# Kernel tuning notes

Hardware: AMD Instinct MI355X
Metric: run time of the kernel (lower is better)

## Reference

```python
import jax, jax.numpy as jnp
import numpy as np

SIG = [1, 1, 1, 1, -1]  # Cl(4,1)
NVEC = 5
GA = 1 << NVEC  # 32


def _build_gp_table():
    # Cayley table for the geometric product on blades indexed by bitmask.
    G = np.zeros((GA, GA, GA), np.float32)
    for a in range(GA):
        for b in range(GA):
            s = 0
            t = a >> 1
            while t:
                s += bin(t & b).count('1')
                t >>= 1
            sign = -1.0 if (s & 1) else 1.0
            common = a & b
            for i in range(NVEC):
                if (common >> i) & 1:
                    sign *= SIG[i]
            G[a, b, a ^ b] = sign
    return G

GP_TABLE = jnp.asarray(_build_gp_table())


def geometric_product(x, y):
    return jnp.einsum('...i,...j,ijk->...k', x, y, GP_TABLE)


def manifold_norm(x):
    # normalize each multivector onto the unit sphere in R^32
    return x / (jnp.linalg.norm(x, axis=-1, keepdims=True) + 1e-6)


def versor_linear(x, W, b):
    # channel mixing shared across multivector components: x [..., in, ga]
    return jnp.einsum('...ig,oi->...og', x, W) + b


def layer_norm2d(x, w, b):
    # LayerNorm over last two dims [D, ga] jointly
    mu = jnp.mean(x, axis=(-2, -1), keepdims=True)
    var = jnp.var(x, axis=(-2, -1), keepdims=True)
    return (x - mu) / jnp.sqrt(var + 1e-5) * w + b


def attention(x, Wq, bq, Wk, bk, Wv, bv, Wo, bo, n_heads):
    B, S, D, G = x.shape
    dh = D // n_heads
    q = versor_linear(x, Wq, bq).reshape(B, S, n_heads, dh, G)
    k = versor_linear(x, Wk, bk).reshape(B, S, n_heads, dh, G)
    v = versor_linear(x, Wv, bv).reshape(B, S, n_heads, dh, G)
    scale = 1.0 / np.sqrt(dh * G).astype(np.float32)
    scores = jnp.einsum('bshdg,bthdg->bhst', q, k) * scale
    probs = jax.nn.softmax(scores, axis=-1)
    o = jnp.einsum('bhst,bthdg->bshdg', probs, v).reshape(B, S, D, G)
    return versor_linear(o, Wo, bo)


N_HEADS = 8


def forward(x, Wq, bq, Wk, bk, Wv, bv, Wo, bo, ln1_w, ln1_b, ln2_w, ln2_b,
            gamma1, gamma2, W1, b1, W2, b2, Wr, br, Wc, bc):
    L = Wq.shape[0]
    for l in range(L):
        h = attention(layer_norm2d(x, ln1_w[l], ln1_b[l]),
                      Wq[l], bq[l], Wk[l], bk[l], Wv[l], bv[l], Wo[l], bo[l], N_HEADS)
        x = manifold_norm(x + gamma1[l] * h)
        m = versor_linear(layer_norm2d(x, ln2_w[l], ln2_b[l]), W1[l], b1[l])
        m = versor_linear(jnp.tanh(m), W2[l], b2[l])
        x = manifold_norm(x + gamma2[l] * m)
    # RecursiveRotorAccumulator: log(S)-step inclusive scan of rotors
    delta = versor_linear(x, Wr, br)
    rot = 0.5 * delta
    rot = rot.at[..., 0].add(1.0)
    rot = manifold_norm(rot)
    S = x.shape[1]
    step = 1
    while step < S:
        left = rot[:, :-step]
        right = rot[:, step:]
        comb = manifold_norm(geometric_product(right, left))
        rot = jnp.concatenate([rot[:, :step], comb], axis=1)
        step *= 2
    pooled = rot[:, -1]  # [B, D, ga]
    logits = pooled.reshape(pooled.shape[0], -1) @ Wc.T + bc
    return logits


def setup_inputs() -> dict:
    key = jax.random.key(0)
    B, S, D, G, L, NC = 8, 256, 64, GA, 4, 1000
    E = 4 * D  # expansion hidden
    ks = jax.random.split(key, 16)
    sd = 0.02
    inp = {
        'x': jax.random.normal(ks[0], (B, S, D, G), jnp.float32),
        'Wq': jax.random.normal(ks[1], (L, D, D), jnp.float32) * sd,
        'bq': jnp.zeros((L, D, G), jnp.float32),
        'Wk': jax.random.normal(ks[2], (L, D, D), jnp.float32) * sd,
        'bk': jnp.zeros((L, D, G), jnp.float32),
        'Wv': jax.random.normal(ks[3], (L, D, D), jnp.float32) * sd,
        'bv': jnp.zeros((L, D, G), jnp.float32),
        'Wo': jax.random.normal(ks[4], (L, D, D), jnp.float32) * sd,
        'bo': jnp.zeros((L, D, G), jnp.float32),
        'ln1_w': jnp.ones((L, D, G), jnp.float32),
        'ln1_b': jnp.zeros((L, D, G), jnp.float32),
        'ln2_w': jnp.ones((L, D, G), jnp.float32),
        'ln2_b': jnp.zeros((L, D, G), jnp.float32),
        'gamma1': 1e-5 * jnp.ones((L, D, G), jnp.float32),
        'gamma2': 1e-5 * jnp.ones((L, D, G), jnp.float32),
        'W1': jax.random.normal(ks[5], (L, E, D), jnp.float32) * sd,
        'b1': jnp.zeros((L, E, G), jnp.float32),
        'W2': jax.random.normal(ks[6], (L, D, E), jnp.float32) * sd,
        'b2': jnp.zeros((L, D, G), jnp.float32),
        'Wr': jax.random.normal(ks[7], (D, D), jnp.float32) * sd,
        'br': jnp.zeros((D, G), jnp.float32),
        'Wc': jax.random.normal(ks[8], (NC, D * G), jnp.float32) * sd,
        'bc': jnp.zeros((NC,), jnp.float32),
    }
    return inp


def reference(x, Wq, bq, Wk, bk, Wv, bv, Wo, bo, ln1_w, ln1_b, ln2_w, ln2_b,
              gamma1, gamma2, W1, b1, W2, b2, Wr, br, Wc, bc):
    return forward(x, Wq, bq, Wk, bk, Wv, bv, Wo, bo, ln1_w, ln1_b, ln2_w, ln2_b,
                   gamma1, gamma2, W1, b1, W2, b2, Wr, br, Wc, bc)
```

## Files before the change

kernel.cpp:

```cpp
#include <hip/hip_runtime.h>
#include <hip/hip_bf16.h>

constexpr int kB  = 8;
constexpr int kS  = 256;
constexpr int kD  = 64;
constexpr int kG  = 32;
constexpr int kE  = 256;
constexpr int kNH = 8;
constexpr int kHD = 256;
constexpr int kDG = kD * kG;
constexpr int kT  = kB * kS;
constexpr int kNC = 1000;

using bf16x8 = __attribute__((ext_vector_type(8))) short;
using f32x4  = __attribute__((ext_vector_type(4))) float;

__device__ __forceinline__ short f2bf(float f) {
    unsigned u = __float_as_uint(f);
    unsigned r = (u + 0x7FFFu + ((u >> 16) & 1u)) >> 16;
    return (short)r;
}

__device__ __forceinline__ float tanh_fast(float x) {
    float a = fabsf(x);
    float e = __expf(-2.f * a);
    float d = 1.f + e;
    float r = __builtin_amdgcn_rcpf(d);
    r = r * (2.f - d * r);
    float t = (1.f - e) * r;
    return copysignf(t, x);
}

__global__ __launch_bounds__(256) void cvtw_kernel(
    const float* __restrict__ Wq, const float* __restrict__ Wk,
    const float* __restrict__ Wv, const float* __restrict__ Wo,
    const float* __restrict__ W1, const float* __restrict__ W2,
    unsigned short* __restrict__ dst) {
    int idx = (blockIdx.x * 256 + threadIdx.x) * 4;
    const float* src; int off;
    if      (idx <  16384) { src = Wq; off = 0; }
    else if (idx <  32768) { src = Wk; off = 16384; }
    else if (idx <  49152) { src = Wv; off = 32768; }
    else if (idx <  65536) { src = Wo; off = 49152; }
    else if (idx < 131072) { src = W1; off = 65536; }
    else                   { src = W2; off = 131072; }
    const float4 v = *(const float4*)(src + (idx - off));
    *(short4*)&dst[idx] = make_short4(f2bf(v.x), f2bf(v.y), f2bf(v.z), f2bf(v.w));
}

__global__ __launch_bounds__(256) void prep_tr_kernel(
    const float* __restrict__ bq, const float* __restrict__ bk,
    const float* __restrict__ bv, const float* __restrict__ bo,
    const float* __restrict__ b2, const float* __restrict__ gm1,
    const float* __restrict__ gm2, const float* __restrict__ ln2w,
    const float* __restrict__ ln2b, const float* __restrict__ ln1w,
    const float* __restrict__ ln1b, const float* __restrict__ b1,
    float* __restrict__ dst) {
    __shared__ float lt[32 * 257];
    const int a = blockIdx.x >> 2, l = blockIdx.x & 3;
    const float* srcs[12] = {bq, bk, bv, bo, b2, gm1, gm2, ln2w, ln2b, ln1w, ln1b, b1};
    const int R  = (a == 11) ? 256 : 64;
    const int sh = (a == 11) ? 8 : 6;
    const float* src = srcs[a] + (size_t)l * R * 32;
    float* out = dst + a * 8192 + l * R * 32;
    const int tid = threadIdx.x;
    for (int j = tid; j < R * 32; j += 256) lt[(j & 31) * (R + 1) + (j >> 5)] = src[j];
    __syncthreads();
    for (int k = tid; k < R * 32; k += 256) {
        int g = k >> sh, r = k & (R - 1);
        out[k] = lt[g * (R + 1) + r];
    }
}

__global__ __launch_bounds__(256) void ln_kernel(const float* __restrict__ Xin,
                                                 const float* __restrict__ w,
                                                 const float* __restrict__ b,
                                                 unsigned short* __restrict__ A,
                                                 float* __restrict__ XT) {
    int t = blockIdx.x, tid = threadIdx.x;
    const float* xp = Xin + (size_t)t * kDG;
    __shared__ float r1[256], r2[256];
    __shared__ short st[32 * 72];
    __shared__ float xf[32 * 68];
    float v[8], s = 0.f, ss = 0.f;
#pragma unroll
    for (int j = 0; j < 8; j++) {
        float x = xp[tid + j * 256];
        v[j] = x; s += x; ss += x * x;
        int jj = tid + j * 256;
        xf[(jj & 31) * 68 + (jj >> 5)] = x;
    }
    r1[tid] = s; r2[tid] = ss; __syncthreads();
    for (int o = 128; o > 0; o >>= 1) {
        if (tid < o) { r1[tid] += r1[tid + o]; r2[tid] += r2[tid + o]; }
        __syncthreads();
    }
    float mean = r1[0] * (1.f / kDG);
    float var  = r2[0] * (1.f / kDG) - mean * mean;
    float rstd = rsqrtf(var + 1e-5f);
#pragma unroll
    for (int j = 0; j < 8; j++) {
        int jj = tid + j * 256;
        float val = (v[j] - mean) * rstd * w[jj] + b[jj];
        st[(jj & 31) * 72 + (jj >> 5)] = f2bf(val);
    }
    __syncthreads();
    bf16x8 ov = *(const bf16x8*)&st[(tid >> 3) * 72 + (tid & 7) * 8];
    *(bf16x8*)&A[(size_t)t * kDG + tid * 8] = ov;
    const int row = tid >> 3, col = (tid & 7) * 8;
    float* xo = XT + (size_t)t * kDG + tid * 8;
    *(float4*)(xo + 0) = *(const float4*)&xf[row * 68 + col + 0];
    *(float4*)(xo + 4) = *(const float4*)&xf[row * 68 + col + 4];
}

__global__ __launch_bounds__(256) void vlinT_kernel(const float* __restrict__ XT,
                                                    const float* __restrict__ W,
                                                    const float* __restrict__ bias,
                                                    float* __restrict__ OutT) {
    __shared__ float sx[32 * 65];
    __shared__ float sw[kD * kD];
    int t = blockIdx.x, tid = threadIdx.x;
    const float* xp = XT + (size_t)t * kDG;
    for (int j = tid; j < kDG; j += 256) sx[(j >> 6) * 65 + (j & 63)] = xp[j];
    for (int j = tid; j < kD * kD; j += 256) sw[j] = W[j];
    __syncthreads();
    int g = tid & 31, ob = tid >> 5;
    int b = t >> 8, s = t & 255;
    float* op = OutT + ((size_t)b * kD * kS + s) * kG;
    for (int o = ob; o < kD; o += 8) {
        float acc = bias[o * kG + g];
        const float* wr = sw + o * kD;
#pragma unroll
        for (int i = 0; i < kD; i++) acc += wr[i] * sx[g * 65 + i];
        op[(size_t)o * kS * kG + g] = acc;
    }
}

template<bool LAST>
__global__ __launch_bounds__(256, 2) void mega_kernel(
    const unsigned short* __restrict__ O,
    const unsigned short* __restrict__ Woh, const float* __restrict__ boT,
    const float* __restrict__ gm1T,
    const float* __restrict__ ln2wT, const float* __restrict__ ln2bT,
    const unsigned short* __restrict__ W1h, const float* __restrict__ b1T,
    const unsigned short* __restrict__ W2h, const float* __restrict__ b2T,
    const float* __restrict__ gm2T,
    const float* __restrict__ ln1wT, const float* __restrict__ ln1bT,
    float* __restrict__ XT,
    const unsigned short* __restrict__ Wqh, const unsigned short* __restrict__ Wkh,
    const unsigned short* __restrict__ Wvh,
    const float* __restrict__ bqT, const float* __restrict__ bkT,
    const float* __restrict__ bvT,
    unsigned short* __restrict__ Q, unsigned short* __restrict__ K,
    unsigned short* __restrict__ V) {
    constexpr int AS = 72;
    constexpr int MS = 264;
    __shared__ short sA[32 * AS];
    __shared__ short sM[32 * MS];
    __shared__ float sred[8];

    const int tid = threadIdx.x;
    const int w = tid >> 6, lane = tid & 63;
    const int l16 = lane & 15, quad = lane >> 4;
    const int tok = blockIdx.x;
    const size_t tb = (size_t)tok * kDG;
    const int o0 = w * 16 + quad * 4;

    float xv[2][4];
    bf16x8 w1f[8];
    {
        const unsigned short* xp = O + tb;
        bf16x8 bfr[2][2];
#pragma unroll
        for (int c = 0; c < 2; ++c)
#pragma unroll
            for (int nt = 0; nt < 2; ++nt)
                bfr[c][nt] = *(const bf16x8*)&xp[(nt * 16 + l16) * kD + c * 32 + quad * 8];

        f32x4 accW[2];
#pragma unroll
        for (int nt = 0; nt < 2; ++nt) accW[nt] = (f32x4){0.f, 0.f, 0.f, 0.f};
#pragma unroll
        for (int c = 0; c < 2; ++c) {
            bf16x8 afr = *(const bf16x8*)&Woh[(w * 16 + l16) * kD + c * 32 + quad * 8];
#pragma unroll
            for (int nt = 0; nt < 2; ++nt)
                accW[nt] = __builtin_amdgcn_mfma_f32_16x16x32_bf16(afr, bfr[c][nt], accW[nt], 0, 0, 0);
        }

#pragma unroll
        for (int mt = 0; mt < 4; ++mt)
#pragma unroll
            for (int c = 0; c < 2; ++c)
                w1f[mt * 2 + c] = *(const bf16x8*)&W1h[((w * 4 + mt) * 16 + l16) * kD + c * 32 + quad * 8];

        float s = 0.f, ss = 0.f;
        float vv[2][4];
#pragma unroll
        for (int nt = 0; nt < 2; ++nt) {
            int g = nt * 16 + l16;
            const float4 b4 = *(const float4*)&boT[g * kD + o0];
            const float4 g4 = *(const float4*)&gm1T[g * kD + o0];
            const float4 xi = *(const float4*)&XT[tb + g * kD + o0];
#pragma unroll
            for (int r = 0; r < 4; ++r)
                vv[nt][r] = (&xi.x)[r] + (&g4.x)[r] * (accW[nt][r] + (&b4.x)[r]);
        }
#pragma unroll
        for (int r = 0; r < 4; ++r) {
            float sq = vv[0][r] * vv[0][r] + vv[1][r] * vv[1][r];
#pragma unroll
            for (int off = 1; off < 16; off <<= 1) sq += __shfl_xor(sq, off, 64);
            float rn = 1.f / (sqrtf(sq) + 1e-6f);
#pragma unroll
            for (int nt = 0; nt < 2; ++nt) {
                float x = vv[nt][r] * rn;
                xv[nt][r] = x;
                s += x; ss = fmaf(x, x, ss);
            }
        }
#pragma unroll
        for (int off = 1; off < 64; off <<= 1) {
            s += __shfl_xor(s, off, 64); ss += __shfl_xor(ss, off, 64);
        }
        if (lane == 0) { sred[w] = s; sred[4 + w] = ss; }
        __syncthreads();
        float st = sred[0] + sred[1] + sred[2] + sred[3];
        float sst = sred[4] + sred[5] + sred[6] + sred[7];
        float mean = st * (1.f / kDG);
        float var  = sst * (1.f / kDG) - mean * mean;
        float rstd = rsqrtf(var + 1e-5f);
#pragma unroll
        for (int nt = 0; nt < 2; ++nt) {
            int g = nt * 16 + l16;
            const float4 w4 = *(const float4*)&ln2wT[g * kD + o0];
            const float4 b4 = *(const float4*)&ln2bT[g * kD + o0];
            short4 s4;
#pragma unroll
            for (int r = 0; r < 4; ++r)
                (&s4.x)[r] = f2bf((xv[nt][r] - mean) * rstd * (&w4.x)[r] + (&b4.x)[r]);
            *(short4*)&sA[g * AS + o0] = s4;
        }
    }
    __syncthreads();

    bf16x8 w2f[8];
    {
        bf16x8 afrA[2][2];
#pragma unroll
        for (int c = 0; c < 2; ++c)
#pragma unroll
            for (int nt = 0; nt < 2; ++nt)
                afrA[c][nt] = *(const bf16x8*)&sA[(nt * 16 + l16) * AS + c * 32 + quad * 8];

        f32x4 acc1[4][2];
#pragma unroll
        for (int mt = 0; mt < 4; ++mt)
#pragma unroll
            for (int nt = 0; nt < 2; ++nt) acc1[mt][nt] = (f32x4){0.f, 0.f, 0.f, 0.f};
#pragma unroll
        for (int mt = 0; mt < 4; ++mt)
#pragma unroll
            for (int c = 0; c < 2; ++c)
#pragma unroll
                for (int nt = 0; nt < 2; ++nt)
                    acc1[mt][nt] = __builtin_amdgcn_mfma_f32_16x16x32_bf16(w1f[mt * 2 + c], afrA[c][nt], acc1[mt][nt], 0, 0, 0);

#pragma unroll
        for (int c = 0; c < 8; ++c)
            w2f[c] = *(const bf16x8*)&W2h[(w * 16 + l16) * kE + c * 32 + quad * 8];

#pragma unroll
        for (int mt = 0; mt < 4; ++mt)
#pragma unroll
            for (int nt = 0; nt < 2; ++nt) {
                int g = nt * 16 + l16;
                int e0 = (w * 4 + mt) * 16 + quad * 4;
                const float4 b4 = *(const float4*)&b1T[g * kE + e0];
                short4 s4;
#pragma unroll
                for (int r = 0; r < 4; ++r)
                    (&s4.x)[r] = f2bf(tanh_fast(acc1[mt][nt][r] + (&b4.x)[r]));
                *(short4*)&sM[g * MS + e0] = s4;
            }
    }
    __syncthreads();

    f32x4 acc2[2];
#pragma unroll
    for (int nt = 0; nt < 2; ++nt) acc2[nt] = (f32x4){0.f, 0.f, 0.f, 0.f};
#pragma unroll
    for (int c = 0; c < 8; ++c) {
        bf16x8 bq[2];
#pragma unroll
        for (int nt = 0; nt < 2; ++nt)
            bq[nt] = *(const bf16x8*)&sM[(nt * 16 + l16) * MS + c * 32 + quad * 8];
#pragma unroll
        for (int nt = 0; nt < 2; ++nt)
            acc2[nt] = __builtin_amdgcn_mfma_f32_16x16x32_bf16(w2f[c], bq[nt], acc2[nt], 0, 0, 0);
    }

    bf16x8 wqf[6];
    if constexpr (!LAST) {
        const unsigned short* Wp[3] = {Wqh, Wkh, Wvh};
#pragma unroll
        for (int m = 0; m < 3; ++m)
#pragma unroll
            for (int c = 0; c < 2; ++c)
                wqf[m * 2 + c] = *(const bf16x8*)&Wp[m][(w * 16 + l16) * kD + c * 32 + quad * 8];
    }

    float yv[2][4];
    float s2 = 0.f, ss2 = 0.f;
    {
        float vv[2][4];
#pragma unroll
        for (int nt = 0; nt < 2; ++nt) {
            int g = nt * 16 + l16;
            const float4 b4 = *(const float4*)&b2T[g * kD + o0];
            const float4 g4 = *(const float4*)&gm2T[g * kD + o0];
#pragma unroll
            for (int r = 0; r < 4; ++r)
                vv[nt][r] = xv[nt][r] + (&g4.x)[r] * (acc2[nt][r] + (&b4.x)[r]);
        }
#pragma unroll
        for (int r = 0; r < 4; ++r) {
            float sq = vv[0][r] * vv[0][r] + vv[1][r] * vv[1][r];
#pragma unroll
            for (int off = 1; off < 16; off <<= 1) sq += __shfl_xor(sq, off, 64);
            float rn = 1.f / (sqrtf(sq) + 1e-6f);
#pragma unroll
            for (int nt = 0; nt < 2; ++nt) {
                float x = vv[nt][r] * rn;
                yv[nt][r] = x;
                s2 += x; ss2 = fmaf(x, x, ss2);
            }
        }
#pragma unroll
        for (int nt = 0; nt < 2; ++nt) {
            int g = nt * 16 + l16;
            float4 xo;
#pragma unroll
            for (int r = 0; r < 4; ++r) (&xo.x)[r] = yv[nt][r];
            *(float4*)&XT[tb + g * kD + o0] = xo;
        }
    }
    if constexpr (LAST) return;

#pragma unroll
    for (int off = 1; off < 64; off <<= 1) {
        s2 += __shfl_xor(s2, off, 64); ss2 += __shfl_xor(ss2, off, 64);
    }
    if (lane == 0) { sred[w] = s2; sred[4 + w] = ss2; }
    __syncthreads();
    {
        float st = sred[0] + sred[1] + sred[2] + sred[3];
        float sst = sred[4] + sred[5] + sred[6] + sred[7];
        float mean = st * (1.f / kDG);
        float var  = sst * (1.f / kDG) - mean * mean;
        float rstd = rsqrtf(var + 1e-5f);
#pragma unroll
        for (int nt = 0; nt < 2; ++nt) {
            int g = nt * 16 + l16;
            const float4 w4 = *(const float4*)&ln1wT[g * kD + o0];
            const float4 b4 = *(const float4*)&ln1bT[g * kD + o0];
            short4 s4;
#pragma unroll
            for (int r = 0; r < 4; ++r)
                (&s4.x)[r] = f2bf((yv[nt][r] - mean) * rstd * (&w4.x)[r] + (&b4.x)[r]);
            *(short4*)&sA[g * AS + o0] = s4;
        }
    }
    __syncthreads();

    {
        bf16x8 afrA[2][2];
#pragma unroll
        for (int c = 0; c < 2; ++c)
#pragma unroll
            for (int nt = 0; nt < 2; ++nt)
                afrA[c][nt] = *(const bf16x8*)&sA[(nt * 16 + l16) * AS + c * 32 + quad * 8];

        const float* Bp[3] = {bqT, bkT, bvT};
        unsigned short* Op[3] = {Q, K, V};
#pragma unroll
        for (int m = 0; m < 3; ++m) {
            f32x4 acc3[2];
#pragma unroll
            for (int nt = 0; nt < 2; ++nt) acc3[nt] = (f32x4){0.f, 0.f, 0.f, 0.f};
#pragma unroll
            for (int c = 0; c < 2; ++c)
#pragma unroll
                for (int nt = 0; nt < 2; ++nt)
                    acc3[nt] = __builtin_amdgcn_mfma_f32_16x16x32_bf16(wqf[m * 2 + c], afrA[c][nt], acc3[nt], 0, 0, 0);
            unsigned short* op = Op[m] + tb;
#pragma unroll
            for (int nt = 0; nt < 2; ++nt) {
                int g = nt * 16 + l16;
                const float4 b4 = *(const float4*)&Bp[m][g * kD + o0];
#pragma unroll
                for (int r = 0; r < 4; ++r)
                    op[(o0 + r) * kG + g] = (unsigned short)f2bf(acc3[nt][r] + (&b4.x)[r]);
            }
        }
    }
}

__global__ __launch_bounds__(256, 3) void gemm_qkv_kernel(
    const unsigned short* __restrict__ X,
    const unsigned short* __restrict__ Wqh, const unsigned short* __restrict__ Wkh,
    const unsigned short* __restrict__ Wvh,
    const float* __restrict__ bqT, const float* __restrict__ bkT, const float* __restrict__ bvT,
    unsigned short* __restrict__ Q, unsigned short* __restrict__ K, unsigned short* __restrict__ V) {
    constexpr int WS = 64 + 8;
    __shared__ short sW[3 * 64 * WS];

    const int tid = threadIdx.x, wave = tid >> 6, lane = tid & 63;
    const int l16 = lane & 15, quad = lane >> 4;
    const int tok = blockIdx.x * 4 + wave;

    const unsigned short* Wp[3] = {Wqh, Wkh, Wvh};
#pragma unroll
    for (int w = 0; w < 3; ++w)
        for (int j = tid * 8; j < 64 * 64; j += 2048) {
            int o = j >> 6, i = j & 63;
            *(bf16x8*)&sW[w * 64 * WS + o * WS + i] = *(const bf16x8*)(Wp[w] + j);
        }

    const unsigned short* xp = X + (size_t)tok * kDG;
    bf16x8 bfr[2][2];
#pragma unroll
    for (int c = 0; c < 2; ++c)
#pragma unroll
        for (int nt = 0; nt < 2; ++nt)
            bfr[c][nt] = *(const bf16x8*)&xp[(nt * 16 + l16) * kD + c * 32 + quad * 8];
    __syncthreads();

    f32x4 acc[3][4][2];
#pragma unroll
    for (int w = 0; w < 3; ++w)
#pragma unroll
        for (int mt = 0; mt < 4; ++mt)
#pragma unroll
            for (int nt = 0; nt < 2; ++nt) acc[w][mt][nt] = (f32x4){0.f, 0.f, 0.f, 0.f};

#pragma unroll
    for (int w = 0; w < 3; ++w)
#pragma unroll
        for (int mt = 0; mt < 4; ++mt)
#pragma unroll
            for (int c = 0; c < 2; ++c) {
                bf16x8 afr = *(const bf16x8*)&sW[w * 64 * WS + (mt * 16 + l16) * WS + c * 32 + quad * 8];
#pragma unroll
                for (int nt = 0; nt < 2; ++nt)
                    acc[w][mt][nt] = __builtin_amdgcn_mfma_f32_16x16x32_bf16(afr, bfr[c][nt], acc[w][mt][nt], 0, 0, 0);
            }

    unsigned short* Op[3] = {Q, K, V};
    const float* Bp[3] = {bqT, bkT, bvT};
#pragma unroll
    for (int w = 0; w < 3; ++w) {
        unsigned short* op = Op[w] + (size_t)tok * kDG;
#pragma unroll
        for (int mt = 0; mt < 4; ++mt)
#pragma unroll
            for (int nt = 0; nt < 2; ++nt) {
                int g = nt * 16 + l16;
                int o0 = mt * 16 + quad * 4;
                const float4 b4 = *(const float4*)&Bp[w][g * kD + o0];
#pragma unroll
                for (int r = 0; r < 4; ++r)
                    op[(o0 + r) * kG + g] = (unsigned short)f2bf(acc[w][mt][nt][r] + (&b4.x)[r]);
            }
    }
}

constexpr int QSTR = 264;
constexpr int VSTR = 40;

__global__ __launch_bounds__(128) void attn_mfma_kernel(const unsigned short* __restrict__ Q,
                                                        const unsigned short* __restrict__ K,
                                                        const unsigned short* __restrict__ V,
                                                        unsigned short* __restrict__ O) {
    __shared__ short sQ[32 * QSTR];
    __shared__ short sKV[2][256 * VSTR];

    const int qt = blockIdx.x, h = blockIdx.y, b = blockIdx.z;
    const int tid = threadIdx.x;
    const int wave = tid >> 6, lane = tid & 63;
    const int l16 = lane & 15, quad = lane >> 4;

    const size_t bh = (size_t)b * kS * kDG + (size_t)h * kHD;

#pragma unroll
    for (int it = 0; it < 8; ++it) {
        int j = it * 1024 + tid * 8;
        int row = j >> 8, col = j & 255;
        *(bf16x8*)&sQ[row * QSTR + col] =
            *(const bf16x8*)(Q + bh + (size_t)(qt * 32 + row) * kDG + col);
    }
#pragma unroll
    for (int it = 0; it < 8; ++it) {
        int j = it * 1024 + tid * 8;
        int row = j >> 8, col = j & 255;
        *(bf16x8*)&sKV[0][row * QSTR + col] =
            *(const bf16x8*)(K + bh + (size_t)row * kDG + col);
    }
    __syncthreads();

    bf16x8 afrag[8];
    {
        int row = wave * 16 + l16;
#pragma unroll
        for (int c = 0; c < 8; ++c)
            afrag[c] = *(const bf16x8*)&sQ[row * QSTR + c * 32 + quad * 8];
    }

    f32x4 acc[16];
#pragma unroll
    for (int i = 0; i < 16; ++i) acc[i] = (f32x4){0.f, 0.f, 0.f, 0.f};

    for (int kt = 0; kt < 8; ++kt) {
        bf16x8 kpre[8];
        if (kt < 7) {
#pragma unroll
            for (int it = 0; it < 8; ++it) {
                int j = it * 1024 + tid * 8;
                int row = j >> 8, col = j & 255;
                kpre[it] = *(const bf16x8*)(K + bh + (size_t)((kt + 1) * 32 + row) * kDG + col);
            }
        }
        const short* kb = sKV[kt & 1];
#pragma unroll
        for (int nt = 0; nt < 2; ++nt) {
            int key = nt * 16 + l16;
            f32x4 a = acc[kt * 2 + nt];
#pragma unroll
            for (int c = 0; c < 8; ++c) {
                bf16x8 bfrag = *(const bf16x8*)&kb[key * QSTR + c * 32 + quad * 8];
                a = __builtin_amdgcn_mfma_f32_16x16x32_bf16(afrag[c], bfrag, a, 0, 0, 0);
            }
            acc[kt * 2 + nt] = a;
        }
        if (kt < 7) {
            short* nb = sKV[(kt + 1) & 1];
#pragma unroll
            for (int it = 0; it < 8; ++it) {
                int j = it * 1024 + tid * 8;
                int row = j >> 8, col = j & 255;
                *(bf16x8*)&nb[row * QSTR + col] = kpre[it];
            }
            __syncthreads();
        }
    }

    float inv[4];
#pragma unroll
    for (int r = 0; r < 4; ++r) {
        float m = -1e30f;
#pragma unroll
        for (int t = 0; t < 16; ++t) m = fmaxf(m, acc[t][r]);
#pragma unroll
        for (int off = 1; off < 16; off <<= 1) m = fmaxf(m, __shfl_xor(m, off, 16));
        float s = 0.f;
#pragma unroll
        for (int t = 0; t < 16; ++t) {
            float p = __expf((acc[t][r] - m) * 0.0625f);
            acc[t][r] = p; s += p;
        }
#pragma unroll
        for (int off = 1; off < 16; off <<= 1) s += __shfl_xor(s, off, 16);
        inv[r] = 1.f / s;
    }

#pragma unroll
    for (int t = 0; t < 16; ++t)
#pragma unroll
        for (int r = 0; r < 4; ++r)
            sQ[(wave * 16 + quad * 4 + r) * QSTR + t * 16 + l16] = f2bf(acc[t][r]);

    {
        const int db = tid & 63, kh = tid >> 6;
        short4 vr[16];
#pragma unroll
        for (int r = 0; r < 16; ++r)
            vr[r] = *(const short4*)(V + bh + (size_t)(kh * 16 + r) * kDG + db * 4);
#pragma unroll
        for (int i = 0; i < 4; ++i)
#pragma unroll
            for (int gq = 0; gq < 4; ++gq) {
                short4 p = make_short4((&vr[gq * 4 + 0].x)[i], (&vr[gq * 4 + 1].x)[i],
                                       (&vr[gq * 4 + 2].x)[i], (&vr[gq * 4 + 3].x)[i]);
                *(short4*)&sKV[0][(db * 4 + i) * VSTR + kh * 16 + gq * 4] = p;
            }
    }
    __syncthreads();

    f32x4 oacc[16];
#pragma unroll
    for (int i = 0; i < 16; ++i) oacc[i] = (f32x4){0.f, 0.f, 0.f, 0.f};

    for (int vt = 0; vt < 8; ++vt) {
        short4 vpre[16];
        if (vt < 7) {
            const int db = tid & 63, kh = tid >> 6;
#pragma unroll
            for (int r = 0; r < 16; ++r)
                vpre[r] = *(const short4*)(V + bh + (size_t)((vt + 1) * 32 + kh * 16 + r) * kDG + db * 4);
        }
        const short* vb = sKV[vt & 1];
        bf16x8 pfrag = *(const bf16x8*)&sQ[(wave * 16 + l16) * QSTR + vt * 32 + quad * 8];
#pragma unroll
        for (int dt = 0; dt < 16; ++dt) {
            bf16x8 vfrag = *(const bf16x8*)&vb[(dt * 16 + l16) * VSTR + quad * 8];
            oacc[dt] = __builtin_amdgcn_mfma_f32_16x16x32_bf16(pfrag, vfrag, oacc[dt], 0, 0, 0);
        }
        if (vt < 7) {
            const int db = tid & 63, kh = tid >> 6;
            short* nb = sKV[(vt + 1) & 1];
#pragma unroll
            for (int i = 0; i < 4; ++i)
#pragma unroll
                for (int gq = 0; gq < 4; ++gq) {
                    short4 p = make_short4((&vpre[gq * 4 + 0].x)[i], (&vpre[gq * 4 + 1].x)[i],
                                           (&vpre[gq * 4 + 2].x)[i], (&vpre[gq * 4 + 3].x)[i]);
                    *(short4*)&nb[(db * 4 + i) * VSTR + kh * 16 + gq * 4] = p;
                }
            __syncthreads();
        }
    }

    {
        const size_t ob = (size_t)(b * kS + qt * 32 + wave * 16 + quad * 4) * kDG + h * 8;
#pragma unroll
        for (int gg = 0; gg < 2; ++gg) {
            int g = gg * 16 + l16;
#pragma unroll
            for (int r = 0; r < 4; ++r) {
                bf16x8 pk;
#pragma unroll
                for (int k = 0; k < 8; ++k)
                    pk[k] = f2bf(oacc[k * 2 + gg][r] * inv[r]);
                *(bf16x8*)&O[ob + (size_t)r * kDG + g * kD] = pk;
            }
        }
    }
}

constexpr int pc_ce(unsigned v) { int c = 0; while (v) { c += v & 1; v >>= 1; } return c; }
constexpr unsigned gp_mask_ce(int a) {
    unsigned m = 0;
    for (int c = 0; c < 32; ++c) {
        int b = a ^ c;
        int s = (a & b) >> 4;
        for (int t = a >> 1; t; t >>= 1) s += pc_ce(t & b);
        if (s & 1) m |= (1u << c);
    }
    return m;
}

template<int A>
__device__ __forceinline__ void gp_term(const float* x, const float* y, float* acc) {
    constexpr unsigned m = gp_mask_ce(A);
    const float xa = x[A], nxa = -xa;
#pragma unroll
    for (int c = 0; c < 32; ++c)
        acc[c] = fmaf(((m >> c) & 1u) ? nxa : xa, y[A ^ c], acc[c]);
}

__device__ __forceinline__ void gp_mn_t(const float* x, const float* y, float* out) {
    float acc[32];
#pragma unroll
    for (int c = 0; c < 32; ++c) acc[c] = 0.f;
    gp_term<0>(x, y, acc);  gp_term<1>(x, y, acc);  gp_term<2>(x, y, acc);  gp_term<3>(x, y, acc);
    gp_term<4>(x, y, acc);  gp_term<5>(x, y, acc);  gp_term<6>(x, y, acc);  gp_term<7>(x, y, acc);
    gp_term<8>(x, y, acc);  gp_term<9>(x, y, acc);  gp_term<10>(x, y, acc); gp_term<11>(x, y, acc);
    gp_term<12>(x, y, acc); gp_term<13>(x, y, acc); gp_term<14>(x, y, acc); gp_term<15>(x, y, acc);
    gp_term<16>(x, y, acc); gp_term<17>(x, y, acc); gp_term<18>(x, y, acc); gp_term<19>(x, y, acc);
    gp_term<20>(x, y, acc); gp_term<21>(x, y, acc); gp_term<22>(x, y, acc); gp_term<23>(x, y, acc);
    gp_term<24>(x, y, acc); gp_term<25>(x, y, acc); gp_term<26>(x, y, acc); gp_term<27>(x, y, acc);
    gp_term<28>(x, y, acc); gp_term<29>(x, y, acc); gp_term<30>(x, y, acc); gp_term<31>(x, y, acc);
    float ss = 0.f;
#pragma unroll
    for (int c = 0; c < 32; ++c) ss = fmaf(acc[c], acc[c], ss);
    float r = 1.f / (sqrtf(ss) + 1e-6f);
#pragma unroll
    for (int c = 0; c < 32; ++c) out[c] = acc[c] * r;
}

__device__ __forceinline__ void leaf_load(const float* base, float* v) {
#pragma unroll
    for (int i = 0; i < 8; ++i) {
        const float4 f = *(const float4*)(base + i * 4);
        v[i * 4 + 0] = 0.5f * f.x; v[i * 4 + 1] = 0.5f * f.y;
        v[i * 4 + 2] = 0.5f * f.z; v[i * 4 + 3] = 0.5f * f.w;
    }
    v[0] += 1.f;
    float ss = 0.f;
#pragma unroll
    for (int c = 0; c < 32; ++c) ss = fmaf(v[c], v[c], ss);
    float r = 1.f / (sqrtf(ss) + 1e-6f);
#pragma unroll
    for (int c = 0; c < 32; ++c) v[c] *= r;
}

__global__ __launch_bounds__(256) void scanreg_kernel(const float* __restrict__ DT,
                                                      float* __restrict__ pooled) {
    const int wave = threadIdx.x >> 6, lane = threadIdx.x & 63;
    const int seq = blockIdx.x * 4 + wave;
    const float* base = DT + ((size_t)seq * kS + lane * 4) * kG;

    float R[32], Y[32], P[32], Xa[32], Yb[32];

    leaf_load(base, R);
    for (int j = 1; j < 4; ++j) {
        leaf_load(base + j * kG, Y);
        gp_mn_t(Y, R, R);
    }

    for (int step = 1; step < 64; step <<= 1) {
        const bool up = lane & step;
#pragma unroll
        for (int c = 0; c < 32; ++c) P[c] = __shfl_xor(R[c], step, 64);
#pragma unroll
        for (int c = 0; c < 32; ++c) {
            Xa[c] = up ? R[c] : P[c];
            Yb[c] = up ? P[c] : R[c];
        }
        gp_mn_t(Xa, Yb, R);
    }

    if (lane == 0) {
        float* op = pooled + (size_t)seq * kG;
#pragma unroll
        for (int i = 0; i < 8; ++i)
            *(float4*)(op + i * 4) = make_float4(R[i * 4], R[i * 4 + 1], R[i * 4 + 2], R[i * 4 + 3]);
    }
}

__global__ __launch_bounds__(256) void cls2_kernel(const float* __restrict__ P,
                                                   const float* __restrict__ Wc,
                                                   const float* __restrict__ bc,
                                                   float* __restrict__ out) {
    __shared__ float sp[kB * kDG];
    const int tid = threadIdx.x, wave = tid >> 6, lane = tid & 63;
    for (int j = tid * 4; j < kB * kDG; j += 1024)
        *(float4*)&sp[j] = *(const float4*)(P + j);
    __syncthreads();

    const int c = blockIdx.x * 4 + wave;
    const float* w = Wc + (size_t)c * kDG;
    float acc[kB];
#pragma unroll
    for (int b = 0; b < kB; ++b) acc[b] = 0.f;
#pragma unroll
    for (int cc = 0; cc < 8; ++cc) {
        const float4 w4 = *(const float4*)(w + cc * 256 + lane * 4);
#pragma unroll
        for (int b = 0; b < kB; ++b) {
            const float4 p4 = *(const float4*)&sp[b * kDG + cc * 256 + lane * 4];
            acc[b] += w4.x * p4.x + w4.y * p4.y + w4.z * p4.z + w4.w * p4.w;
        }
    }
#pragma unroll
    for (int b = 0; b < kB; ++b)
#pragma unroll
        for (int off = 32; off > 0; off >>= 1) acc[b] += __shfl_xor(acc[b], off, 64);
    if (lane == 0) {
        float bias = bc[c];
#pragma unroll
        for (int b = 0; b < kB; ++b) out[b * kNC + c] = acc[b] + bias;
    }
}

extern "C" void kernel_launch(void* const* d_in, const int* in_sizes, int n_in,
                              void* d_out, int out_size, void* d_ws, size_t ws_size,
                              hipStream_t stream) {
    const float* x_in = (const float*)d_in[0];
    const float* Wq   = (const float*)d_in[1];
    const float* bq   = (const float*)d_in[2];
    const float* Wk   = (const float*)d_in[3];
    const float* bk   = (const float*)d_in[4];
    const float* Wv   = (const float*)d_in[5];
    const float* bv   = (const float*)d_in[6];
    const float* Wo   = (const float*)d_in[7];
    const float* bo   = (const float*)d_in[8];
    const float* ln1w = (const float*)d_in[9];
    const float* ln1b = (const float*)d_in[10];
    const float* ln2w = (const float*)d_in[11];
    const float* ln2b = (const float*)d_in[12];
    const float* gm1  = (const float*)d_in[13];
    const float* gm2  = (const float*)d_in[14];
    const float* W1   = (const float*)d_in[15];
    const float* b1   = (const float*)d_in[16];
    const float* W2   = (const float*)d_in[17];
    const float* b2   = (const float*)d_in[18];
    const float* Wr   = (const float*)d_in[19];
    const float* br   = (const float*)d_in[20];
    const float* Wc   = (const float*)d_in[21];
    const float* bc   = (const float*)d_in[22];

    const size_t NEL = (size_t)kT * kDG;
    float* F  = (float*)d_ws;
    float* XT = F;
    unsigned short* Abf = (unsigned short*)(F + NEL);
    unsigned short* Qh = (unsigned short*)(F + 2 * NEL);
    unsigned short* Kh = (unsigned short*)(F + 3 * NEL);
    unsigned short* Vh = (unsigned short*)(F + 4 * NEL);
    unsigned short* Wb = (unsigned short*)(F + 5 * NEL);
    float* PT = F + 3 * NEL + NEL / 2;
    float* pooled = F + 2 * NEL;
    float* DT = F + NEL;

    cvtw_kernel<<<192, 256, 0, stream>>>(Wq, Wk, Wv, Wo, W1, W2, Wb);
    prep_tr_kernel<<<48, 256, 0, stream>>>(bq, bk, bv, bo, b2, gm1, gm2,
                                           ln2w, ln2b, ln1w, ln1b, b1, PT);
    unsigned short* Wqh = Wb;
    unsigned short* Wkh = Wb + 16384;
    unsigned short* Wvh = Wb + 32768;
    unsigned short* Woh = Wb + 49152;
    unsigned short* W1h = Wb + 65536;
    unsigned short* W2h = Wb + 131072;

    auto bqT   = [&](int l) { return PT + 0     + l * 2048; };
    auto bkT   = [&](int l) { return PT + 8192  + l * 2048; };
    auto bvT   = [&](int l) { return PT + 16384 + l * 2048; };
    auto boT   = [&](int l) { return PT + 24576 + l * 2048; };
    auto b2T   = [&](int l) { return PT + 32768 + l * 2048; };
    auto gm1T  = [&](int l) { return PT + 40960 + l * 2048; };
    auto gm2T  = [&](int l) { return PT + 49152 + l * 2048; };
    auto ln2wT = [&](int l) { return PT + 57344 + l * 2048; };
    auto ln2bT = [&](int l) { return PT + 65536 + l * 2048; };
    auto ln1wT = [&](int l) { return PT + 73728 + l * 2048; };
    auto ln1bT = [&](int l) { return PT + 81920 + l * 2048; };
    auto b1T   = [&](int l) { return PT + 90112 + l * 8192; };

    ln_kernel<<<kT, 256, 0, stream>>>(x_in, ln1w, ln1b, Abf, XT);
    gemm_qkv_kernel<<<kT / 4, 256, 0, stream>>>(Abf,
        Wqh, Wkh, Wvh, bqT(0), bkT(0), bvT(0), Qh, Kh, Vh);

    for (int l = 0; l < 4; l++) {
        attn_mfma_kernel<<<dim3(8, kNH, kB), 128, 0, stream>>>(Qh, Kh, Vh, Abf);
        if (l < 3)
            mega_kernel<false><<<kT, 256, 0, stream>>>(Abf,
                Woh + l * 4096, boT(l), gm1T(l), ln2wT(l), ln2bT(l),
                W1h + l * 16384, b1T(l), W2h + l * 16384, b2T(l), gm2T(l),
                ln1wT(l + 1), ln1bT(l + 1), XT,
                Wqh + (l + 1) * 4096, Wkh + (l + 1) * 4096, Wvh + (l + 1) * 4096,
                bqT(l + 1), bkT(l + 1), bvT(l + 1), Qh, Kh, Vh);
        else
            mega_kernel<true><<<kT, 256, 0, stream>>>(Abf,
                Woh + l * 4096, boT(l), gm1T(l), ln2wT(l), ln2bT(l),
                W1h + l * 16384, b1T(l), W2h + l * 16384, b2T(l), gm2T(l),
                nullptr, nullptr, XT,
                nullptr, nullptr, nullptr, nullptr, nullptr, nullptr,
                nullptr, nullptr, nullptr);
    }

    vlinT_kernel<<<kT, 256, 0, stream>>>(XT, Wr, br, DT);
    scanreg_kernel<<<kB * kD / 4, 256, 0, stream>>>(DT, pooled);
    cls2_kernel<<<kNC / 4, 256, 0, stream>>>(pooled, Wc, bc, (float*)d_out);
}
```

Before: 518.8 us.

## Split attention keys across waves with softmax merge; one-wave scan blocks

The attention kernel now handles 16 queries per block instead of 32 and launches twice as many blocks. Each of the two waves processes its own half of the keys, with per-wave K/V staging and no block barriers inside the loops. The two waves' partial results are combined at the end with a log-sum-exp style rescale exchanged through shared memory. The scan kernel is relaunched as one 64-thread block per sequence instead of four waves per block. The aim is more parallelism and fewer barriers, at the cost of reloading Q per block and an extra merge step.

```diff
diff --git a/kernel.cpp b/kernel.cpp
--- a/kernel.cpp
+++ b/kernel.cpp
@@ -475,163 +475,187 @@
     }
 }
 
-constexpr int QSTR = 264;
-constexpr int VSTR = 40;
+constexpr int QS5 = 264;
+constexpr int PS5 = 136;
+constexpr int VS5 = 40;
 
 __global__ __launch_bounds__(128) void attn_mfma_kernel(const unsigned short* __restrict__ Q,
                                                         const unsigned short* __restrict__ K,
                                                         const unsigned short* __restrict__ V,
                                                         unsigned short* __restrict__ O) {
-    __shared__ short sQ[32 * QSTR];
-    __shared__ short sKV[2][256 * VSTR];
+    __shared__ short sQ[16 * QS5];
+    __shared__ short sP[2][16 * PS5];
+    __shared__ short sV[2][128 * VS5];
+    __shared__ float sms[2][2][16];
 
     const int qt = blockIdx.x, h = blockIdx.y, b = blockIdx.z;
     const int tid = threadIdx.x;
-    const int wave = tid >> 6, lane = tid & 63;
+    const int w = tid >> 6, lane = tid & 63;
     const int l16 = lane & 15, quad = lane >> 4;
-
     const size_t bh = (size_t)b * kS * kDG + (size_t)h * kHD;
-
-#pragma unroll
-    for (int it = 0; it < 8; ++it) {
+    const int kb0 = w * 128;
+
+#pragma unroll
+    for (int it = 0; it < 4; ++it) {
         int j = it * 1024 + tid * 8;
         int row = j >> 8, col = j & 255;
-        *(bf16x8*)&sQ[row * QSTR + col] =
-            *(const bf16x8*)(Q + bh + (size_t)(qt * 32 + row) * kDG + col);
-    }
+        *(bf16x8*)&sQ[row * QS5 + col] =
+            *(const bf16x8*)(Q + bh + (size_t)(qt * 16 + row) * kDG + col);
+    }
+    short* kbW = &sV[w][0];
 #pragma unroll
     for (int it = 0; it < 8; ++it) {
-        int j = it * 1024 + tid * 8;
+        int j = it * 512 + lane * 8;
         int row = j >> 8, col = j & 255;
-        *(bf16x8*)&sKV[0][row * QSTR + col] =
-            *(const bf16x8*)(K + bh + (size_t)row * kDG + col);
+        *(bf16x8*)&kbW[row * QS5 + col] =
+            *(const bf16x8*)(K + bh + (size_t)(kb0 + row) * kDG + col);
     }
     __syncthreads();
 
     bf16x8 afrag[8];
-    {
-        int row = wave * 16 + l16;
-#pragma unroll
-        for (int c = 0; c < 8; ++c)
-            afrag[c] = *(const bf16x8*)&sQ[row * QSTR + c * 32 + quad * 8];
-    }
-
-    f32x4 acc[16];
-#pragma unroll
-    for (int i = 0; i < 16; ++i) acc[i] = (f32x4){0.f, 0.f, 0.f, 0.f};
+#pragma unroll
+    for (int c = 0; c < 8; ++c)
+        afrag[c] = *(const bf16x8*)&sQ[l16 * QS5 + c * 32 + quad * 8];
+
+    f32x4 acc[8];
+#pragma unroll
+    for (int i = 0; i < 8; ++i) acc[i] = (f32x4){0.f, 0.f, 0.f, 0.f};
 
     for (int kt = 0; kt < 8; ++kt) {
         bf16x8 kpre[8];
         if (kt < 7) {
 #pragma unroll
             for (int it = 0; it < 8; ++it) {
-                int j = it * 1024 + tid * 8;
+                int j = it * 512 + lane * 8;
                 int row = j >> 8, col = j & 255;
-                kpre[it] = *(const bf16x8*)(K + bh + (size_t)((kt + 1) * 32 + row) * kDG + col);
-            }
-        }
-        const short* kb = sKV[kt & 1];
-#pragma unroll
-        for (int nt = 0; nt < 2; ++nt) {
-            int key = nt * 16 + l16;
-            f32x4 a = acc[kt * 2 + nt];
-#pragma unroll
-            for (int c = 0; c < 8; ++c) {
-                bf16x8 bfrag = *(const bf16x8*)&kb[key * QSTR + c * 32 + quad * 8];
-                a = __builtin_amdgcn_mfma_f32_16x16x32_bf16(afrag[c], bfrag, a, 0, 0, 0);
-            }
-            acc[kt * 2 + nt] = a;
-        }
+                kpre[it] = *(const bf16x8*)(K + bh + (size_t)(kb0 + (kt + 1) * 16 + row) * kDG + col);
+            }
+        }
+        f32x4 a = acc[kt];
+#pragma unroll
+        for (int c = 0; c < 8; ++c) {
+            bf16x8 bfrag = *(const bf16x8*)&kbW[l16 * QS5 + c * 32 + quad * 8];
+            a = __builtin_amdgcn_mfma_f32_16x16x32_bf16(afrag[c], bfrag, a, 0, 0, 0);
+        }
+        acc[kt] = a;
         if (kt < 7) {
-            short* nb = sKV[(kt + 1) & 1];
 #pragma unroll
             for (int it = 0; it < 8; ++it) {
-                int j = it * 1024 + tid * 8;
+                int j = it * 512 + lane * 8;
                 int row = j >> 8, col = j & 255;
-                *(bf16x8*)&nb[row * QSTR + col] = kpre[it];
-            }
-            __syncthreads();
-        }
-    }
-
-    float inv[4];
+                *(bf16x8*)&kbW[row * QS5 + col] = kpre[it];
+            }
+        }
+    }
+
+    float mw[4], sw[4];
 #pragma unroll
     for (int r = 0; r < 4; ++r) {
         float m = -1e30f;
 #pragma unroll
-        for (int t = 0; t < 16; ++t) m = fmaxf(m, acc[t][r]);
+        for (int t = 0; t < 8; ++t) m = fmaxf(m, acc[t][r]);
 #pragma unroll
         for (int off = 1; off < 16; off <<= 1) m = fmaxf(m, __shfl_xor(m, off, 16));
         float s = 0.f;
 #pragma unroll
-        for (int t = 0; t < 16; ++t) {
+        for (int t = 0; t < 8; ++t) {
             float p = __expf((acc[t][r] - m) * 0.0625f);
             acc[t][r] = p; s += p;
         }
 #pragma unroll
         for (int off = 1; off < 16; off <<= 1) s += __shfl_xor(s, off, 16);
-        inv[r] = 1.f / s;
-    }
-
-#pragma unroll
-    for (int t = 0; t < 16; ++t)
+        mw[r] = m; sw[r] = s;
+    }
+
+    short* sPw = &sP[w][0];
+#pragma unroll
+    for (int t = 0; t < 8; ++t)
 #pragma unroll
         for (int r = 0; r < 4; ++r)
-            sQ[(wave * 16 + quad * 4 + r) * QSTR + t * 16 + l16] = f2bf(acc[t][r]);
-
+            sPw[(quad * 4 + r) * PS5 + t * 16 + l16] = f2bf(acc[t][r]);
+
+    short* vbW = &sV[w][0];
+    const int k4 = lane >> 3, dseg = (lane & 7) * 16;
     {
-        const int db = tid & 63, kh = tid >> 6;
-        short4 vr[16];
-#pragma unroll
-        for (int r = 0; r < 16; ++r)
-            vr[r] = *(const short4*)(V + bh + (size_t)(kh * 16 + r) * kDG + db * 4);
-#pragma unroll
-        for (int i = 0; i < 4; ++i)
-#pragma unroll
-            for (int gq = 0; gq < 4; ++gq) {
-                short4 p = make_short4((&vr[gq * 4 + 0].x)[i], (&vr[gq * 4 + 1].x)[i],
-                                       (&vr[gq * 4 + 2].x)[i], (&vr[gq * 4 + 3].x)[i]);
-                *(short4*)&sKV[0][(db * 4 + i) * VSTR + kh * 16 + gq * 4] = p;
-            }
-    }
-    __syncthreads();
+        short4 vr[4][4];
+#pragma unroll
+        for (int r = 0; r < 4; ++r)
+#pragma unroll
+            for (int i = 0; i < 4; ++i)
+                vr[r][i] = *(const short4*)(V + bh + (size_t)(kb0 + k4 * 4 + r) * kDG + dseg + i * 4);
+#pragma unroll
+        for (int i = 0; i < 16; ++i) {
+            short4 p4 = make_short4((&vr[0][i >> 2].x)[i & 3], (&vr[1][i >> 2].x)[i & 3],
+                                    (&vr[2][i >> 2].x)[i & 3], (&vr[3][i >> 2].x)[i & 3]);
+            *(short4*)&vbW[(dseg + i) * VS5 + k4 * 4] = p4;
+        }
+    }
 
     f32x4 oacc[16];
 #pragma unroll
     for (int i = 0; i < 16; ++i) oacc[i] = (f32x4){0.f, 0.f, 0.f, 0.f};
 
-    for (int vt = 0; vt < 8; ++vt) {
-        short4 vpre[16];
-        if (vt < 7) {
-            const int db = tid & 63, kh = tid >> 6;
-#pragma unroll
-            for (int r = 0; r < 16; ++r)
-                vpre[r] = *(const short4*)(V + bh + (size_t)((vt + 1) * 32 + kh * 16 + r) * kDG + db * 4);
-        }
-        const short* vb = sKV[vt & 1];
-        bf16x8 pfrag = *(const bf16x8*)&sQ[(wave * 16 + l16) * QSTR + vt * 32 + quad * 8];
-#pragma unroll
-        for (int dt = 0; dt < 16; ++dt) {
-            bf16x8 vfrag = *(const bf16x8*)&vb[(dt * 16 + l16) * VSTR + quad * 8];
-            oacc[dt] = __builtin_amdgcn_mfma_f32_16x16x32_bf16(pfrag, vfrag, oacc[dt], 0, 0, 0);
-        }
-        if (vt < 7) {
-            const int db = tid & 63, kh = tid >> 6;
-            short* nb = sKV[(vt + 1) & 1];
-#pragma unroll
-            for (int i = 0; i < 4; ++i)
-#pragma unroll
-                for (int gq = 0; gq < 4; ++gq) {
-                    short4 p = make_short4((&vpre[gq * 4 + 0].x)[i], (&vpre[gq * 4 + 1].x)[i],
-                                           (&vpre[gq * 4 + 2].x)[i], (&vpre[gq * 4 + 3].x)[i]);
-                    *(short4*)&nb[(db * 4 + i) * VSTR + kh * 16 + gq * 4] = p;
-                }
-            __syncthreads();
-        }
-    }
-
-    {
-        const size_t ob = (size_t)(b * kS + qt * 32 + wave * 16 + quad * 4) * kDG + h * 8;
+    for (int t = 0; t < 8; ++t) {
+        const int dh = t >> 2, vt = t & 3;
+        short4 vpre[4][4];
+        if (t < 7) {
+            const int nt_ = t + 1, ndh = nt_ >> 2, nvt = nt_ & 3;
+#pragma unroll
+            for (int r = 0; r < 4; ++r)
+#pragma unroll
+                for (int i = 0; i < 4; ++i)
+                    vpre[r][i] = *(const short4*)(V + bh + (size_t)(kb0 + nvt * 32 + k4 * 4 + r) * kDG + ndh * 128 + dseg + i * 4);
+        }
+        bf16x8 pfrag = *(const bf16x8*)&sPw[l16 * PS5 + vt * 32 + quad * 8];
+#pragma unroll
+        for (int dt = 0; dt < 8; ++dt) {
+            bf16x8 vfrag = *(const bf16x8*)&vbW[(dt * 16 + l16) * VS5 + quad * 8];
+            oacc[dh * 8 + dt] = __builtin_amdgcn_mfma_f32_16x16x32_bf16(pfrag, vfrag, oacc[dh * 8 + dt], 0, 0, 0);
+        }
+        if (t < 7) {
+#pragma unroll
+            for (int i = 0; i < 16; ++i) {
+                short4 p4 = make_short4((&vpre[0][i >> 2].x)[i & 3], (&vpre[1][i >> 2].x)[i & 3],
+                                        (&vpre[2][i >> 2].x)[i & 3], (&vpre[3][i >> 2].x)[i & 3]);
+                *(short4*)&vbW[(dseg + i) * VS5 + k4 * 4] = p4;
+            }
+        }
+    }
+
+    if (l16 == 0) {
+#pragma unroll
+        for (int r = 0; r < 4; ++r) {
+            sms[w][0][quad * 4 + r] = mw[r];
+            sms[w][1][quad * 4 + r] = sw[r];
+        }
+    }
+    __syncthreads();
+
+    float cs[4], inv[4];
+#pragma unroll
+    for (int r = 0; r < 4; ++r) {
+        float mo = sms[1 - w][0][quad * 4 + r];
+        float so = sms[1 - w][1][quad * 4 + r];
+        float M = fmaxf(mw[r], mo);
+        cs[r] = __expf((mw[r] - M) * 0.0625f);
+        float co = __expf((mo - M) * 0.0625f);
+        inv[r] = 1.f / (sw[r] * cs[r] + so * co);
+    }
+
+    float* mbuf = (float*)&sV[0][0];
+    if (w == 1) {
+#pragma unroll
+        for (int od = 0; od < 16; ++od) {
+            int d = (od >> 3) * 128 + (od & 7) * 16 + l16;
+#pragma unroll
+            for (int r = 0; r < 4; ++r)
+                mbuf[(quad * 4 + r) * 260 + d] = oacc[od][r] * cs[r];
+        }
+    }
+    __syncthreads();
+
+    if (w == 0) {
+        const size_t ob = (size_t)(b * kS + qt * 16 + quad * 4) * kDG + h * 8;
 #pragma unroll
         for (int gg = 0; gg < 2; ++gg) {
             int g = gg * 16 + l16;
@@ -639,8 +663,12 @@
             for (int r = 0; r < 4; ++r) {
                 bf16x8 pk;
 #pragma unroll
-                for (int k = 0; k < 8; ++k)
-                    pk[k] = f2bf(oacc[k * 2 + gg][r] * inv[r]);
+                for (int k = 0; k < 8; ++k) {
+                    int od = (k >> 2) * 8 + (k & 3) * 2 + gg;
+                    int d = (od >> 3) * 128 + (od & 7) * 16 + l16;
+                    float mrg = oacc[od][r] * cs[r] + mbuf[(quad * 4 + r) * 260 + d];
+                    pk[k] = f2bf(mrg * inv[r]);
+                }
                 *(bf16x8*)&O[ob + (size_t)r * kDG + g * kD] = pk;
             }
         }
@@ -704,10 +732,10 @@
     for (int c = 0; c < 32; ++c) v[c] *= r;
 }
 
-__global__ __launch_bounds__(256) void scanreg_kernel(const float* __restrict__ DT,
-                                                      float* __restrict__ pooled) {
-    const int wave = threadIdx.x >> 6, lane = threadIdx.x & 63;
-    const int seq = blockIdx.x * 4 + wave;
+__global__ __launch_bounds__(64) void scanreg_kernel(const float* __restrict__ DT,
+                                                     float* __restrict__ pooled) {
+    const int lane = threadIdx.x & 63;
+    const int seq = blockIdx.x;
     const float* base = DT + ((size_t)seq * kS + lane * 4) * kG;
 
     float R[32], Y[32], P[32], Xa[32], Yb[32];
@@ -840,7 +868,7 @@
         Wqh, Wkh, Wvh, bqT(0), bkT(0), bvT(0), Qh, Kh, Vh);
 
     for (int l = 0; l < 4; l++) {
-        attn_mfma_kernel<<<dim3(8, kNH, kB), 128, 0, stream>>>(Qh, Kh, Vh, Abf);
+        attn_mfma_kernel<<<dim3(16, kNH, kB), 128, 0, stream>>>(Qh, Kh, Vh, Abf);
         if (l < 3)
             mega_kernel<false><<<kT, 256, 0, stream>>>(Abf,
                 Woh + l * 4096, boT(l), gm1T(l), ln2wT(l), ln2bT(l),
@@ -858,6 +886,6 @@
     }
 
     vlinT_kernel<<<kT, 256, 0, stream>>>(XT, Wr, br, DT);
-    scanreg_kernel<<<kB * kD / 4, 256, 0, stream>>>(DT, pooled);
+    scanreg_kernel<<<kB * kD, 64, 0, stream>>>(DT, pooled);
     cls2_kernel<<<kNC / 4, 256, 0, stream>>>(pooled, Wc, bc, (float*)d_out);
 }
```

Result: slower. 536.3 us (+3.4%).
